# Kernel tuning notes

Hardware: AMD Instinct MI355X
Metric: run time of the kernel (lower is better)

Reference implementation:

```python
import jax, jax.numpy as jnp
import numpy as np

B, Tc, E, K, M, V = 8, 1024, 256, 8, 2048, 16
T1 = Tc * K          # penultimate layer length = 8192
TLAST = M * K        # last layer length = 16384


def setup_inputs() -> dict:
    key = jax.random.key(0)
    ks = jax.random.split(key, 12)
    x = jax.random.normal(ks[0], (B, Tc, E), jnp.float32)
    # penultimate values: exactly M 'mixed' tokens (value==2) per row, rest in {1,3}
    base = jnp.where(jnp.arange(T1) < M, 2, 1 + 2 * jax.random.randint(ks[1], (B, T1), 0, 2))
    perm = jnp.argsort(jax.random.uniform(ks[2], (B, T1)), axis=1)
    val1 = jnp.take_along_axis(base, perm, axis=1)
    vallast = 1 + 2 * jax.random.randint(ks[3], (B, TLAST), 0, 2)
    value = jnp.concatenate([val1, vallast], axis=1).astype(jnp.int64)
    depth = jnp.concatenate([jnp.full((B, T1), 5), jnp.full((B, TLAST), 6)], axis=1).astype(jnp.int64)
    pos = jax.random.randint(ks[4], (B, T1 + TLAST, 3), 0, 64).astype(jnp.int64)
    s = 0.02
    W1 = s * jax.random.normal(ks[5], (E, E, K), jnp.float32)  # ConvTranspose1d weight [in,out,k]
    b1 = s * jax.random.normal(ks[6], (E,), jnp.float32)
    W0 = s * jax.random.normal(ks[7], (E, E, K), jnp.float32)
    b0 = s * jax.random.normal(ks[8], (E,), jnp.float32)
    Wl = s * jax.random.normal(ks[9], (V + 1, E), jnp.float32)
    bl = s * jax.random.normal(ks[10], (V + 1,), jnp.float32)
    return {"x": x, "value": value, "depth": depth, "pos": pos, "num_mix": M,
            "W1": W1, "b1": b1, "W0": W0, "b0": b0, "Wl": Wl, "bl": bl}


def _deconv(x, W, b):
    # ConvTranspose1d with kernel=stride=K: each token expands to K tokens
    n, t, e = x.shape
    o = W.shape[1]
    y = jnp.einsum('nte,eoj->ntjo', x, W)  # [N,T,K,O]
    return y.reshape(n, t * W.shape[2], o) + b


def reference(x, value, depth, pos, num_mix, W1, b1, W0, b0, Wl, bl):
    n, tc, e = x.shape
    k = W1.shape[2]
    t1 = tc * k
    max_depth = jnp.max(depth)
    len_1 = jnp.sum(depth == max_depth - 1, axis=1)               # [N]
    tt = jnp.arange(t1)
    val_1 = jnp.where(tt[None, :] < len_1[:, None], value[:, :t1], 0)  # padded penultimate values
    mix_mask = val_1 == 2                                         # [N,T1]
    mix_1 = jnp.sum(mix_mask, axis=1)                             # [N]
    y_1 = _deconv(x, W1, b1)                                      # [N,T1,E]
    # stable pack: bring positions with value==2 to the front, keep order
    order = jnp.argsort(jnp.where(mix_mask, 0, 1), axis=1, stable=True)
    sel = order[:, :num_mix]                                      # [N,M]
    x_0 = jnp.take_along_axis(y_1, sel[:, :, None], axis=1)       # [N,M,E]
    valid = (jnp.arange(num_mix)[None, :] < mix_1[:, None]).astype(x_0.dtype)
    x_0 = x_0 * valid[:, :, None]                                 # zero-pad beyond per-row mix count
    y_0 = _deconv(x_0, W0, b0)                                    # [N,M*K,E]
    return y_0 @ Wl.T + bl                                        # [N,M*K,V+1]
```

## Files before the change

### kernel.cpp

```cpp
#include <hip/hip_runtime.h>

typedef __attribute__((ext_vector_type(8))) short bf16x8;
typedef __attribute__((ext_vector_type(4))) float f32x4;

#define BB 8
#define TC 1024
#define EE 256
#define KJ 8
#define MSEL 2048
#define V1 17
#define T1 8192
#define TTOT 24576
#define BI_TOT 16384
#define NCOLP 160
#define WSTRIDE 264

#define SCAL_OFF 0
#define GRP_OFF  1024
#define WFT_OFF  (GRP_OFF + 524288)
#define B2_OFF   (WFT_OFF + NCOLP*WSTRIDE*2)
#define BF0_OFF  (B2_OFF + 640)
#define WCT_OFF  (BF0_OFF + 128)

__device__ __forceinline__ unsigned short f2bf(float f) {
    union { float f; unsigned u; } x; x.f = f;
    unsigned r = x.u + 0x7fffu + ((x.u >> 16) & 1u);
    return (unsigned short)(r >> 16);
}
__device__ __forceinline__ float bf2f(unsigned short h) {
    union { unsigned u; float f; } x; x.u = ((unsigned)h) << 16;
    return x.f;
}

__device__ __forceinline__ float blockReduceSum256(float v) {
    __shared__ float sm[4];
    #pragma unroll
    for (int d = 32; d; d >>= 1) v += __shfl_down(v, d, 64);
    int lane = threadIdx.x & 63, wid = threadIdx.x >> 6;
    if (lane == 0) sm[wid] = v;
    __syncthreads();
    float r = sm[0] + sm[1] + sm[2] + sm[3];
    __syncthreads();
    return r;
}

__global__ __launch_bounds__(256) void k_pre(const float* W0, const float* Wl, const int* depth,
                                             unsigned short* wfT, int* scal) {
    int bid = blockIdx.x, tid = threadIdx.x;
    __shared__ float w0s[EE * KJ];
    __shared__ float wls[V1 * 257];
    __shared__ int s_red[4];
    if (bid < 256) {
        int em = bid;
        for (int idx = tid; idx < EE * KJ; idx += 256) w0s[idx] = W0[em * EE * KJ + idx];
        for (int idx = tid; idx < V1 * EE; idx += 256) {
            int v = idx >> 8, o = idx & 255;
            wls[v * 257 + o] = Wl[idx];
        }
        __syncthreads();
        if (tid < 136) {
            int j = tid / V1, v = tid - j * V1;
            float acc = 0.f;
            #pragma unroll 4
            for (int o = 0; o < EE; ++o) acc += w0s[o * KJ + j] * wls[v * 257 + o];
            wfT[(j * 20 + v) * WSTRIDE + em] = f2bf(acc);
        }
    } else {
        int b = bid - 256;
        if (b == 0 && tid < 8) scal[33 + tid] = 0;
        const int4* dp = (const int4*)(depth + b * TTOT);
        int m = -2147483648;
        for (int i = tid; i < 6144; i += 256) {
            int4 d = dp[i];
            m = max(max(m, max(d.x, d.y)), max(d.z, d.w));
        }
        #pragma unroll
        for (int dd = 32; dd; dd >>= 1) m = max(m, __shfl_down(m, dd, 64));
        if ((tid & 63) == 0) s_red[tid >> 6] = m;
        __syncthreads();
        int bmax = max(max(s_red[0], s_red[1]), max(s_red[2], s_red[3]));
        if (tid == 0) { atomicMax(&scal[0], bmax); scal[1 + b] = bmax; }
        int c1 = 0, c2 = 0;
        for (int i = tid; i < 6144; i += 256) {
            int4 d = dp[i];
            c1 += (d.x == bmax) + (d.y == bmax) + (d.z == bmax) + (d.w == bmax);
            c2 += (d.x == bmax - 1) + (d.y == bmax - 1) + (d.z == bmax - 1) + (d.w == bmax - 1);
        }
        int cc = (c1 << 16) + c2;
        #pragma unroll
        for (int dd = 32; dd; dd >>= 1) cc += __shfl_down(cc, dd, 64);
        __syncthreads();
        if ((tid & 63) == 0) s_red[tid >> 6] = cc;
        __syncthreads();
        if (tid == 0) {
            int tot = s_red[0] + s_red[1] + s_red[2] + s_red[3];
            scal[9 + b] = tot >> 16;
            scal[17 + b] = tot & 0xffff;
        }
    }
}

__global__ __launch_bounds__(256) void k_mid(
        const int* value, const float* W1, const float* b1, const float* b0,
        const float* Wl, const float* bl,
        int* scal, int* groups, const unsigned short* wfT, float* bias2, float* bf0,
        unsigned short* wct) {
    int bid = blockIdx.x, tid = threadIdx.x;
    __shared__ union {
        struct { unsigned short b1s[32 * WSTRIDE]; unsigned short af[NCOLP * 72]; } w;
    } sm;
    __shared__ int s_wt[4], s_lcnt[8], s_lcnt2[8], s_lbase[8];
    if (bid < 64) {
        int g = bid >> 3;
        int e0 = (bid & 7) * 32;
        unsigned short* b1s = sm.w.b1s;
        unsigned short* af = sm.w.af;
        {
            int em_l = tid & 63;
            int eb = (tid >> 6) * 8;
            #pragma unroll
            for (int i = 0; i < 8; ++i) {
                int e = eb + i;
                #pragma unroll
                for (int c = 0; c < 4; ++c) {
                    int em = c * 64 + em_l;
                    b1s[e * WSTRIDE + em] = f2bf(W1[(e0 + e) * (EE * KJ) + em * KJ + g]);
                }
            }
        }
        for (int idx = tid; idx < 1280; idx += 256) {
            int row = idx >> 3, f = idx & 7;
            ((int4*)af)[row * 9 + f] = ((const int4*)wfT)[row * 33 + f];
        }
        __syncthreads();

        int w = tid >> 6, l = tid & 63;
        int ntile = w & 1, mhalf = w >> 1;
        int lr = l & 15, lq = l >> 4;
        f32x4 acc[5];
        #pragma unroll
        for (int t = 0; t < 5; ++t) acc[t] = (f32x4){0.f, 0.f, 0.f, 0.f};

        for (int ch = 0; ch < 4; ++ch) {
            if (ch) {
                __syncthreads();
                for (int idx = tid; idx < 1280; idx += 256) {
                    int row = idx >> 3, f = idx & 7;
                    ((int4*)af)[row * 9 + f] = ((const int4*)wfT)[row * 33 + ch * 8 + f];
                }
                __syncthreads();
            }
            #pragma unroll
            for (int s = 0; s < 2; ++s) {
                bf16x8 bfr = *(const bf16x8*)&b1s[(ntile * 16 + lr) * WSTRIDE + ch * 64 + s * 32 + lq * 8];
                #pragma unroll
                for (int t = 0; t < 5; ++t) {
                    bf16x8 afr = *(const bf16x8*)&af[((mhalf * 5 + t) * 16 + lr) * 72 + s * 32 + lq * 8];
                    acc[t] = __builtin_amdgcn_mfma_f32_16x16x32_bf16(afr, bfr, acc[t], 0, 0, 0);
                }
            }
        }
        #pragma unroll
        for (int t = 0; t < 5; ++t) {
            int m = (mhalf * 5 + t) * 16 + lq * 4;
            int n = e0 + ntile * 16 + lr;
            #pragma unroll
            for (int r = 0; r < 4; ++r)
                wct[(g * NCOLP + m + r) * WSTRIDE + n] = f2bf(acc[t][r]);
        }
    } else if (bid < 72) {
        int b = bid - 64;
        int gmax = scal[0];
        int mb = scal[1 + b], cm = scal[9 + b], cm1 = scal[17 + b];
        int len1 = (mb == gmax) ? cm1 : ((mb == gmax - 1) ? cm : 0);
        const int* vb = value + b * TTOT;
        int t0 = tid * 32;
        unsigned mask = 0;
        #pragma unroll
        for (int k = 0; k < 32; k += 4) {
            int4 v = *(const int4*)(vb + t0 + k);
            if (t0 + k + 0 < len1 && v.x == 2) mask |= 1u << (k + 0);
            if (t0 + k + 1 < len1 && v.y == 2) mask |= 1u << (k + 1);
            if (t0 + k + 2 < len1 && v.z == 2) mask |= 1u << (k + 2);
            if (t0 + k + 3 < len1 && v.w == 2) mask |= 1u << (k + 3);
        }
        int cnt = __popc(mask);
        int inc = cnt;
        #pragma unroll
        for (int d = 1; d < 64; d <<= 1) {
            int n = __shfl_up(inc, d, 64);
            if ((tid & 63) >= d) inc += n;
        }
        int lane = tid & 63, wid = tid >> 6;
        if (lane == 63) s_wt[wid] = inc;
        if (tid < 8) { s_lcnt[tid] = 0; s_lcnt2[tid] = 0; }
        __syncthreads();
        int woff = 0;
        for (int w = 0; w < wid; ++w) woff += s_wt[w];
        int off0 = woff + inc - cnt;
        int mix1 = s_wt[0] + s_wt[1] + s_wt[2] + s_wt[3];
        int mix1c = min(mix1, MSEL);
        {
            int off = off0;
            #pragma unroll
            for (int k = 0; k < 32; ++k) {
                if (mask & (1u << k)) {
                    if (off < MSEL) atomicAdd(&s_lcnt[(t0 + k) & 7], 1);
                    off++;
                }
            }
        }
        if (tid == 0 && mix1c < MSEL) atomicAdd(&s_lcnt[0], MSEL - mix1c);
        __syncthreads();
        if (tid < 8) s_lbase[tid] = atomicAdd(&scal[33 + tid], s_lcnt[tid]);
        __syncthreads();
        {
            int off = off0;
            #pragma unroll
            for (int k = 0; k < 32; ++k) {
                if (mask & (1u << k)) {
                    if (off < MSEL) {
                        int t = t0 + k;
                        int g = t & 7;
                        int ls = atomicAdd(&s_lcnt2[g], 1);
                        groups[g * BI_TOT + s_lbase[g] + ls] =
                            ((b * MSEL + off) << 11) | ((t >> 3) << 1) | 1;
                    }
                    off++;
                }
            }
        }
        for (int i = mix1c + tid; i < MSEL; i += 256) {
            int ls = atomicAdd(&s_lcnt2[0], 1);
            groups[s_lbase[0] + ls] = (b * MSEL + i) << 11;
        }
    } else if (bid < 89) {
        int v = bid - 72;
        float s = blockReduceSum256(b0[tid] * Wl[v * EE + tid]);
        if (tid == 0) bf0[v] = s + bl[v];
    } else {
        #pragma unroll
        for (int r = 0; r < 2; ++r) {
            int c17 = (bid - 89) * 2 + r;
            int j = c17 / V1, v = c17 - j * V1;
            int colP = j * 20 + v;
            float s = blockReduceSum256(b1[tid] * bf2f(wfT[colP * WSTRIDE + tid]));
            if (tid == 0) bias2[colP] = s;
        }
    }
}

__global__ __launch_bounds__(256) void k_main(const float* x, const unsigned short* wct,
        const int* scal, const int* groups, const float* bias2, const float* bf0, float* out) {
    int g = blockIdx.x >> 7;
    int tile0 = blockIdx.x & 127;
    int cntg = scal[33 + g];

    __shared__ __align__(16) unsigned short xs[32 * WSTRIDE];
    __shared__ __align__(16) unsigned short wts[NCOLP * 72];
    __shared__ int xoffs[32], obase[32];
    __shared__ unsigned char vflag[32];
    int tid = threadIdx.x;
    const int4* wsrc = (const int4*)wct;

    for (int tile = tile0; tile * 32 < cntg; tile += 128) {
        int nrows = min(32, cntg - tile * 32);
        __syncthreads();
        if (tid < 32) {
            int flag = 0, xo = 0, ob = 0;
            if (tid < nrows) {
                int p = groups[g * BI_TOT + tile * 32 + tid];
                int valid = p & 1;
                int tq = (p >> 1) & 1023;
                int bi = p >> 11;
                int b = bi >> 11;
                xo = (b * TC + tq) * EE;
                ob = bi * 136;
                flag = 1 + valid;
            }
            xoffs[tid] = xo; obase[tid] = ob; vflag[tid] = (unsigned char)flag;
        }
        __syncthreads();
        {
            int row = tid >> 3, q = tid & 7;
            const float* xp = x + xoffs[row];
            #pragma unroll
            for (int i = 0; i < 8; ++i) {
                int f4 = q + 8 * i;
                float4 v = *(const float4*)(xp + f4 * 4);
                ushort4 pk;
                pk.x = f2bf(v.x); pk.y = f2bf(v.y); pk.z = f2bf(v.z); pk.w = f2bf(v.w);
                *(ushort4*)&xs[row * WSTRIDE + f4 * 4] = pk;
            }
        }
        for (int idx = tid; idx < 1280; idx += 256) {
            int row = idx >> 3, f = idx & 7;
            ((int4*)wts)[row * 9 + f] = wsrc[(g * NCOLP + row) * 33 + f];
        }
        __syncthreads();

        int w = tid >> 6, l = tid & 63;
        int rw = w & 1, chalf = w >> 1;
        int lr = l & 15, lq = l >> 4;
        f32x4 acc[5];
        #pragma unroll
        for (int t = 0; t < 5; ++t) acc[t] = (f32x4){0.f, 0.f, 0.f, 0.f};

        for (int ch = 0; ch < 4; ++ch) {
            if (ch) {
                __syncthreads();
                for (int idx = tid; idx < 1280; idx += 256) {
                    int row = idx >> 3, f = idx & 7;
                    ((int4*)wts)[row * 9 + f] = wsrc[(g * NCOLP + row) * 33 + ch * 8 + f];
                }
                __syncthreads();
            }
            #pragma unroll
            for (int s = 0; s < 2; ++s) {
                bf16x8 afr = *(const bf16x8*)&xs[(rw * 16 + lr) * WSTRIDE + ch * 64 + s * 32 + lq * 8];
                #pragma unroll
                for (int t = 0; t < 5; ++t) {
                    bf16x8 bfr = *(const bf16x8*)&wts[((chalf * 5 + t) * 16 + lr) * 72 + s * 32 + lq * 8];
                    acc[t] = __builtin_amdgcn_mfma_f32_16x16x32_bf16(afr, bfr, acc[t], 0, 0, 0);
                }
            }
        }
        #pragma unroll
        for (int t = 0; t < 5; ++t) {
            int col = (chalf * 5 + t) * 16 + lr;
            int j = col / 20, v = col % 20;
            if (v < V1) {
                float bb = bias2[col] + bf0[v];
                float b0v = bf0[v];
                #pragma unroll
                for (int r = 0; r < 4; ++r) {
                    int row = rw * 16 + lq * 4 + r;
                    int fl = vflag[row];
                    if (fl) out[obase[row] + j * V1 + v] = (fl == 2) ? (acc[t][r] + bb) : b0v;
                }
            }
        }
    }
}

extern "C" void kernel_launch(void* const* d_in, const int* in_sizes, int n_in,
                              void* d_out, int out_size, void* d_ws, size_t ws_size,
                              hipStream_t stream) {
    const float* x     = (const float*)d_in[0];
    const int*   value = (const int*)d_in[1];
    const int*   depth = (const int*)d_in[2];
    const float* W1    = (const float*)d_in[5];
    const float* b1    = (const float*)d_in[6];
    const float* W0    = (const float*)d_in[7];
    const float* b0    = (const float*)d_in[8];
    const float* Wl    = (const float*)d_in[9];
    const float* bl    = (const float*)d_in[10];
    float* out = (float*)d_out;
    char* ws = (char*)d_ws;

    int*            scal   = (int*)(ws + SCAL_OFF);
    int*            groups = (int*)(ws + GRP_OFF);
    unsigned short* wfT    = (unsigned short*)(ws + WFT_OFF);
    float*          bias2  = (float*)(ws + B2_OFF);
    float*          bf0    = (float*)(ws + BF0_OFF);
    unsigned short* wct    = (unsigned short*)(ws + WCT_OFF);

    k_pre <<<dim3(264),  dim3(256), 0, stream>>>(W0, Wl, depth, wfT, scal);
    k_mid <<<dim3(157),  dim3(256), 0, stream>>>(value, W1, b1, b0, Wl, bl,
                                                 scal, groups, wfT, bias2, bf0, wct);
    k_main<<<dim3(1024), dim3(256), 0, stream>>>(x, wct, scal, groups, bias2, bf0, out);
}
```

Before: 115.3 us.

## Move bias folding into k_pre and halve k_main grid to 512 blocks

The bias2 and bf0 folded-bias computations move from k_mid into extra blocks of k_pre. bias2 is now computed in fp32 directly from W0 and Wl instead of from the bf16 wfT, which slightly changes numerics. k_mid shrinks to 72 blocks, and k_main drops from 1024 to 512 blocks, so each block loops over more tiles per group. This cuts tail work in the middle kernel and per-block setup in the main kernel, at the risk of less parallelism in k_main.

```diff
diff --git a/kernel.cpp b/kernel.cpp
--- a/kernel.cpp
+++ b/kernel.cpp
@@ -9,7 +9,6 @@
 #define KJ 8
 #define MSEL 2048
 #define V1 17
-#define T1 8192
 #define TTOT 24576
 #define BI_TOT 16384
 #define NCOLP 160
@@ -27,47 +26,33 @@
     unsigned r = x.u + 0x7fffu + ((x.u >> 16) & 1u);
     return (unsigned short)(r >> 16);
 }
-__device__ __forceinline__ float bf2f(unsigned short h) {
-    union { unsigned u; float f; } x; x.u = ((unsigned)h) << 16;
-    return x.f;
-}
-
-__device__ __forceinline__ float blockReduceSum256(float v) {
-    __shared__ float sm[4];
-    #pragma unroll
-    for (int d = 32; d; d >>= 1) v += __shfl_down(v, d, 64);
-    int lane = threadIdx.x & 63, wid = threadIdx.x >> 6;
-    if (lane == 0) sm[wid] = v;
-    __syncthreads();
-    float r = sm[0] + sm[1] + sm[2] + sm[3];
-    __syncthreads();
-    return r;
-}
 
 __global__ __launch_bounds__(256) void k_pre(const float* W0, const float* Wl, const int* depth,
-                                             unsigned short* wfT, int* scal) {
+                                             const float* b1, const float* b0, const float* bl,
+                                             unsigned short* wfT, float* bias2, float* bf0, int* scal) {
     int bid = blockIdx.x, tid = threadIdx.x;
-    __shared__ float w0s[EE * KJ];
-    __shared__ float wls[V1 * 257];
+    __shared__ union {
+        struct { float w0s[EE * KJ]; float wls[V1 * 257]; } a;
+        struct { float b1v[EE]; float tmp[EE]; } bias;
+    } sm;
     __shared__ int s_red[4];
     if (bid < 256) {
         int em = bid;
-        for (int idx = tid; idx < EE * KJ; idx += 256) w0s[idx] = W0[em * EE * KJ + idx];
+        for (int idx = tid; idx < EE * KJ; idx += 256) sm.a.w0s[idx] = W0[em * EE * KJ + idx];
         for (int idx = tid; idx < V1 * EE; idx += 256) {
             int v = idx >> 8, o = idx & 255;
-            wls[v * 257 + o] = Wl[idx];
+            sm.a.wls[v * 257 + o] = Wl[idx];
         }
         __syncthreads();
         if (tid < 136) {
             int j = tid / V1, v = tid - j * V1;
             float acc = 0.f;
             #pragma unroll 4
-            for (int o = 0; o < EE; ++o) acc += w0s[o * KJ + j] * wls[v * 257 + o];
+            for (int o = 0; o < EE; ++o) acc += sm.a.w0s[o * KJ + j] * sm.a.wls[v * 257 + o];
             wfT[(j * 20 + v) * WSTRIDE + em] = f2bf(acc);
         }
-    } else {
+    } else if (bid < 264) {
         int b = bid - 256;
-        if (b == 0 && tid < 8) scal[33 + tid] = 0;
         const int4* dp = (const int4*)(depth + b * TTOT);
         int m = -2147483648;
         for (int i = tid; i < 6144; i += 256) {
@@ -97,14 +82,38 @@
             scal[9 + b] = tot >> 16;
             scal[17 + b] = tot & 0xffff;
         }
+    } else if (bid < 272) {
+        int j = bid - 264;
+        sm.bias.b1v[tid] = b1[tid];
+        __syncthreads();
+        const float* wp = W0 + tid * KJ + j;
+        float s = 0.f;
+        #pragma unroll 4
+        for (int e = 0; e < EE; ++e) s += sm.bias.b1v[e] * wp[e * (EE * KJ)];
+        sm.bias.tmp[tid] = s;
+        __syncthreads();
+        if (tid < V1) {
+            float a = 0.f;
+            const float* wlp = Wl + tid * EE;
+            #pragma unroll 4
+            for (int o = 0; o < EE; ++o) a += sm.bias.tmp[o] * wlp[o];
+            bias2[j * 20 + tid] = a;
+        }
+    } else {
+        if (tid < 8) scal[33 + tid] = 0;
+        if (tid < V1) {
+            float a = bl[tid];
+            const float* wlp = Wl + tid * EE;
+            #pragma unroll 4
+            for (int o = 0; o < EE; ++o) a += b0[o] * wlp[o];
+            bf0[tid] = a;
+        }
     }
 }
 
 __global__ __launch_bounds__(256) void k_mid(
-        const int* value, const float* W1, const float* b1, const float* b0,
-        const float* Wl, const float* bl,
-        int* scal, int* groups, const unsigned short* wfT, float* bias2, float* bf0,
-        unsigned short* wct) {
+        const int* value, const float* W1,
+        int* scal, int* groups, const unsigned short* wfT, unsigned short* wct) {
     int bid = blockIdx.x, tid = threadIdx.x;
     __shared__ union {
         struct { unsigned short b1s[32 * WSTRIDE]; unsigned short af[NCOLP * 72]; } w;
@@ -168,7 +177,7 @@
             for (int r = 0; r < 4; ++r)
                 wct[(g * NCOLP + m + r) * WSTRIDE + n] = f2bf(acc[t][r]);
         }
-    } else if (bid < 72) {
+    } else {
         int b = bid - 64;
         int gmax = scal[0];
         int mb = scal[1 + b], cm = scal[9 + b], cm1 = scal[17 + b];
@@ -234,26 +243,13 @@
             int ls = atomicAdd(&s_lcnt2[0], 1);
             groups[s_lbase[0] + ls] = (b * MSEL + i) << 11;
         }
-    } else if (bid < 89) {
-        int v = bid - 72;
-        float s = blockReduceSum256(b0[tid] * Wl[v * EE + tid]);
-        if (tid == 0) bf0[v] = s + bl[v];
-    } else {
-        #pragma unroll
-        for (int r = 0; r < 2; ++r) {
-            int c17 = (bid - 89) * 2 + r;
-            int j = c17 / V1, v = c17 - j * V1;
-            int colP = j * 20 + v;
-            float s = blockReduceSum256(b1[tid] * bf2f(wfT[colP * WSTRIDE + tid]));
-            if (tid == 0) bias2[colP] = s;
-        }
     }
 }
 
 __global__ __launch_bounds__(256) void k_main(const float* x, const unsigned short* wct,
         const int* scal, const int* groups, const float* bias2, const float* bf0, float* out) {
-    int g = blockIdx.x >> 7;
-    int tile0 = blockIdx.x & 127;
+    int g = blockIdx.x >> 6;
+    int tile0 = blockIdx.x & 63;
     int cntg = scal[33 + g];
 
     __shared__ __align__(16) unsigned short xs[32 * WSTRIDE];
@@ -263,7 +259,7 @@
     int tid = threadIdx.x;
     const int4* wsrc = (const int4*)wct;
 
-    for (int tile = tile0; tile * 32 < cntg; tile += 128) {
+    for (int tile = tile0; tile * 32 < cntg; tile += 64) {
         int nrows = min(32, cntg - tile * 32);
         __syncthreads();
         if (tid < 32) {
@@ -365,8 +361,7 @@
     float*          bf0    = (float*)(ws + BF0_OFF);
     unsigned short* wct    = (unsigned short*)(ws + WCT_OFF);
 
-    k_pre <<<dim3(264),  dim3(256), 0, stream>>>(W0, Wl, depth, wfT, scal);
-    k_mid <<<dim3(157),  dim3(256), 0, stream>>>(value, W1, b1, b0, Wl, bl,
-                                                 scal, groups, wfT, bias2, bf0, wct);
-    k_main<<<dim3(1024), dim3(256), 0, stream>>>(x, wct, scal, groups, bias2, bf0, out);
-}
+    k_pre <<<dim3(273), dim3(256), 0, stream>>>(W0, Wl, depth, b1, b0, bl, wfT, bias2, bf0, scal);
+    k_mid <<<dim3(72),  dim3(256), 0, stream>>>(value, W1, scal, groups, wfT, wct);
+    k_main<<<dim3(512), dim3(256), 0, stream>>>(x, wct, scal, groups, bias2, bf0, out);
+}
```

After: 149.3 us. +29.5%, slower.
